# Optimization experiments

Measured on AMD Instinct MI355X. Metric: run time of the kernel, lower is better.

Reference implementation:

```python
import jax, jax.numpy as jnp
import numpy as np

MIN_D, MAX_D = 0.1, 1.0
KSIZE = 5


def gaussian_kernel(ksize):
    sigma = ksize / 6.0
    x = jnp.arange(ksize, dtype=jnp.float32) - ksize // 2
    k1 = jnp.exp(-0.5 * x ** 2 / sigma ** 2)
    k1 = k1 / k1.sum()
    return (k1[:, None] * k1[None, :])[None, None]  # [1,1,k,k]


def setup_inputs() -> dict:
    key = jax.random.key(0)
    k1, k2 = jax.random.split(key)
    B, H, W = 8, 512, 512
    TH = TW = 512
    contrast_map = jax.random.normal(k1, (B, 1, H, W), dtype=jnp.float32)
    # uniform [0,1) randoms replacing the per-sample torch.rand calls
    rand_offsets = jax.random.uniform(k2, (B, TH, TW, 4, 2), dtype=jnp.float32)
    return {
        "contrast_map": contrast_map,
        "rand_offsets": rand_offsets,
        "smoothing_kernel": gaussian_kernel(KSIZE),
        "target_height": TH,
        "target_width": TW,
    }


def reference(contrast_map, rand_offsets, smoothing_kernel, target_height, target_width):
    B, _, H, W = contrast_map.shape
    # per-sample min-max normalization to [0,1]
    mn = contrast_map.min(axis=(1, 2, 3), keepdims=True)
    mx = contrast_map.max(axis=(1, 2, 3), keepdims=True)
    norm = jnp.where(mx > mn, (contrast_map - mn) / (mx - mn), jnp.zeros_like(contrast_map))
    # gaussian smoothing, same padding
    pad = KSIZE // 2
    smoothed = jax.lax.conv_general_dilated(
        norm, smoothing_kernel, window_strides=(1, 1),
        padding=[(pad, pad), (pad, pad)],
        dimension_numbers=("NCHW", "OIHW", "NCHW"))
    # contrast -> density: min_d + (max_d-min_d) * sqrt(c)
    density = MIN_D + (MAX_D - MIN_D) * jnp.sqrt(smoothed)  # [B,1,H,W]

    # nearest-index lookup:  h_idx = floor(i*H/TH) clamped
    hi = jnp.minimum((jnp.arange(target_height) * H) // target_height, H - 1)
    wi = jnp.minimum((jnp.arange(target_width) * W) // target_width, W - 1)
    local = density[:, 0][:, hi][:, :, wi]  # [B,TH,TW]

    # per-pixel sample count: >0.7 -> 4, >0.4 -> 2, else 1
    num_samples = jnp.where(local > 0.7, 4, jnp.where(local > 0.4, 2, 1))  # int [B,TH,TW]

    yb = jnp.linspace(-1.0, 1.0, target_height)
    xb = jnp.linspace(-1.0, 1.0, target_width)
    base = jnp.stack(jnp.broadcast_arrays(yb[:, None], xb[None, :]), axis=-1)  # [TH,TW,2] (y,x)
    cell = jnp.array([2.0 / target_height, 2.0 / target_width], dtype=jnp.float32)
    off = (rand_offsets - 0.5) * cell * 0.8  # [B,TH,TW,4,2]
    use_off = (num_samples > 1)[..., None, None]  # single-sample pixels use the base coord
    coords = base[None, :, :, None, :] + jnp.where(use_off, off, 0.0)  # [B,TH,TW,4,2]

    slot = jnp.arange(4)
    valid = slot[None, None, None, :] < num_samples[..., None]  # [B,TH,TW,4]
    weights = jnp.where(valid, local[..., None] / num_samples[..., None], 0.0)  # [B,TH,TW,4]
    return coords, weights, density
```

## Files before the change

kernel.cpp:

```cpp
#include <hip/hip_runtime.h>

static constexpr int B = 8, Himg = 512, Wimg = 512, TH = 512, TW = 512;
static constexpr int BPB = 32;

typedef float f4 __attribute__((ext_vector_type(4)));
typedef float f2 __attribute__((ext_vector_type(2)));

__global__ __launch_bounds__(256) void minmax_kernel(const float* __restrict__ cm,
                                                     float* __restrict__ wsmin,
                                                     float* __restrict__ wsmax) {
    int b   = blockIdx.x / BPB;
    int blk = blockIdx.x % BPB;
    const f4* p = (const f4*)(cm + (size_t)b * Himg * Wimg);
    float mn = 3.4e38f, mx = -3.4e38f;
    int base = blk * 2048;
    #pragma unroll
    for (int k = 0; k < 8; ++k) {
        f4 v = p[base + k * 256 + threadIdx.x];
        mn = fminf(mn, fminf(fminf(v.x, v.y), fminf(v.z, v.w)));
        mx = fmaxf(mx, fmaxf(fmaxf(v.x, v.y), fmaxf(v.z, v.w)));
    }
    #pragma unroll
    for (int off = 32; off; off >>= 1) {
        mn = fminf(mn, __shfl_xor(mn, off));
        mx = fmaxf(mx, __shfl_xor(mx, off));
    }
    __shared__ float smn[4], smx[4];
    int wave = threadIdx.x >> 6, lane = threadIdx.x & 63;
    if (lane == 0) { smn[wave] = mn; smx[wave] = mx; }
    __syncthreads();
    if (threadIdx.x == 0) {
        mn = fminf(fminf(smn[0], smn[1]), fminf(smn[2], smn[3]));
        mx = fmaxf(fmaxf(smx[0], smx[1]), fmaxf(smx[2], smx[3]));
        wsmin[b * BPB + blk] = mn;
        wsmax[b * BPB + blk] = mx;
    }
}

__global__ __launch_bounds__(256) void fused_kernel(const float* __restrict__ cm,
                                                    const float* __restrict__ kern,
                                                    const float* __restrict__ wsmin,
                                                    const float* __restrict__ wsmax,
                                                    const float* __restrict__ rnd,
                                                    float* __restrict__ coords,
                                                    float* __restrict__ weights,
                                                    float* __restrict__ dens) {
    __shared__ float tile[36][37];
    __shared__ float kf[25];
    __shared__ float dsm[1024];

    int tid = threadIdx.x;
    int b = blockIdx.z;
    int bx = blockIdx.x * 32, by = blockIdx.y * 32;

    if (tid < 25) kf[tid] = kern[tid];

    float mnf = 3.4e38f, mxf = -3.4e38f;
    #pragma unroll
    for (int k = 0; k < BPB; ++k) {
        mnf = fminf(mnf, wsmin[b * BPB + k]);
        mxf = fmaxf(mxf, wsmax[b * BPB + k]);
    }
    bool ok = mxf > mnf;
    double mn = (double)mnf;
    double inv = ok ? (1.0 / ((double)mxf - mn)) : 0.0;
    float mnf32 = mnf;
    float invf32 = (float)inv;

    const float* img = cm + (size_t)b * Himg * Wimg;
    for (int idx = tid; idx < 36 * 36; idx += 256) {
        int r = idx / 36, c = idx % 36;
        int gy = by + r - 2, gx = bx + c - 2;
        float v = 0.0f;
        if (gy >= 0 && gy < Himg && gx >= 0 && gx < Wimg)
            v = ok ? (img[gy * Wimg + gx] - mnf32) * invf32 : 0.0f;
        tile[r][c] = v;
    }
    __syncthreads();

    {
        int ox = tid & 31;
        int oy0 = (tid >> 5) << 2;
        float acc[4] = {0.f, 0.f, 0.f, 0.f};
        #pragma unroll
        for (int yy = 0; yy < 8; ++yy) {
            float rv[5];
            #pragma unroll
            for (int dx = 0; dx < 5; ++dx) rv[dx] = tile[oy0 + yy][ox + dx];
            #pragma unroll
            for (int r = 0; r < 4; ++r) {
                int dy = yy - r;
                if (dy >= 0 && dy < 5) {
                    #pragma unroll
                    for (int dx = 0; dx < 5; ++dx)
                        acc[r] = fmaf(rv[dx], kf[dy * 5 + dx], acc[r]);
                }
            }
        }
        #pragma unroll
        for (int r = 0; r < 4; ++r) {
            int oy = oy0 + r;
            float D32 = 0.1f + 0.9f * sqrtf(fmaxf(acc[r], 0.0f));
            float Dout = D32;
            int code;
            if (fabsf(D32 - 0.7f) < 1e-4f || fabsf(D32 - 0.4f) < 1e-4f) {
                double s64 = 0.0;
                #pragma unroll
                for (int dy = 0; dy < 5; ++dy)
                    for (int dx = 0; dx < 5; ++dx) {
                        int gy = by + oy + dy - 2, gx = bx + ox + dx - 2;
                        double v = 0.0;
                        if (gy >= 0 && gy < Himg && gx >= 0 && gx < Wimg)
                            v = ((double)img[gy * Wimg + gx] - mn) * inv;
                        s64 += v * (double)kern[dy * 5 + dx];
                    }
                double D64 = 0.1 + 0.9 * sqrt(s64);
                code = D64 > 0.7 ? 2 : (D64 > 0.4 ? 1 : 0);
                Dout = (float)D64;
            } else {
                code = D32 > 0.7f ? 2 : (D32 > 0.4f ? 1 : 0);
            }
            unsigned u = (__float_as_uint(Dout) & ~3u) | (unsigned)code;
            float enc = __uint_as_float(u);
            dsm[oy * 32 + ox] = enc;
            dens[(size_t)b * Himg * Wimg + (size_t)(by + oy) * Wimg + (bx + ox)] = enc;
        }
    }
    __syncthreads();

    const float cy = (2.0f / TH) * 0.8f;
    const float cx = (2.0f / TW) * 0.8f;
    int lane = tid & 63, wv = tid >> 6;
    #pragma unroll
    for (int k = 0; k < 8; ++k) {
        int row = k * 4 + wv;
        int gy = by + row;
        int gx = bx + (lane >> 1);
        int h = lane & 1;

        float local = dsm[row * 32 + (lane >> 1)];
        int code = __float_as_uint(local) & 3;
        int num = 1 << code;
        bool useoff = num > 1;

        float yb = -1.0f + gy * (2.0f / (TH - 1));
        float xb = -1.0f + gx * (2.0f / (TW - 1));

        size_t f4i = 2 * ((size_t)b * (Himg * Wimg) + (size_t)gy * Wimg + bx) + lane;
        f4 r = ((const f4*)rnd)[f4i];
        f4 c;
        c.x = yb + (useoff ? (r.x - 0.5f) * cy : 0.0f);
        c.y = xb + (useoff ? (r.y - 0.5f) * cx : 0.0f);
        c.z = yb + (useoff ? (r.z - 0.5f) * cy : 0.0f);
        c.w = xb + (useoff ? (r.w - 0.5f) * cx : 0.0f);
        ((f4*)coords)[f4i] = c;

        float invw = local * __uint_as_float(0x3f800000u - ((unsigned)code << 23));
        f2 w;
        if (h == 0) {
            w.x = invw;
            w.y = (num > 1) ? invw : 0.0f;
        } else {
            float v = (num > 3) ? invw : 0.0f;
            w.x = v;
            w.y = v;
        }
        ((f2*)weights)[f4i] = w;
    }
}

extern "C" void kernel_launch(void* const* d_in, const int* in_sizes, int n_in,
                              void* d_out, int out_size, void* d_ws, size_t ws_size,
                              hipStream_t stream) {
    const float* cm   = (const float*)d_in[0];
    const float* rnd  = (const float*)d_in[1];
    const float* kern = (const float*)d_in[2];
    float* out     = (float*)d_out;
    float* coords  = out;
    float* weights = out + (size_t)B * TH * TW * 8;
    float* dens    = weights + (size_t)B * TH * TW * 4;
    float* wsmin   = (float*)d_ws;
    float* wsmax   = wsmin + B * BPB;

    minmax_kernel<<<B * BPB, 256, 0, stream>>>(cm, wsmin, wsmax);
    dim3 gridF(Wimg / 32, Himg / 32, B);
    fused_kernel<<<gridF, 256, 0, stream>>>(cm, kern, wsmin, wsmax, rnd,
                                            coords, weights, dens);
}
```

Baseline: 49.27 us.

## Split fused kernel into density stencil and flat streaming output kernel

Breaks the fused kernel into a tiled density/stencil kernel that writes the encoded density, and a separate flat 1D kernel that reads density back and streams coords and weights with full-width vector stores. The aim is simpler, fully coalesced, sync-free streaming with better occupancy for the bandwidth-bound output. In exchange it adds a kernel launch and a re-read of the density array from memory or L2.

```diff
diff --git a/kernel.cpp b/kernel.cpp
--- a/kernel.cpp
+++ b/kernel.cpp
@@ -1,10 +1,12 @@
 #include <hip/hip_runtime.h>
 
 static constexpr int B = 8, Himg = 512, Wimg = 512, TH = 512, TW = 512;
+static constexpr int NPIX = B * Himg * Wimg;
 static constexpr int BPB = 32;
+static constexpr int WBLOCKS = NPIX / 256;
+static constexpr int CBLOCKS = 2 * NPIX / 256;
 
 typedef float f4 __attribute__((ext_vector_type(4)));
-typedef float f2 __attribute__((ext_vector_type(2)));
 
 __global__ __launch_bounds__(256) void minmax_kernel(const float* __restrict__ cm,
                                                      float* __restrict__ wsmin,
@@ -37,17 +39,13 @@
     }
 }
 
-__global__ __launch_bounds__(256) void fused_kernel(const float* __restrict__ cm,
-                                                    const float* __restrict__ kern,
-                                                    const float* __restrict__ wsmin,
-                                                    const float* __restrict__ wsmax,
-                                                    const float* __restrict__ rnd,
-                                                    float* __restrict__ coords,
-                                                    float* __restrict__ weights,
-                                                    float* __restrict__ dens) {
+__global__ __launch_bounds__(256) void density_kernel(const float* __restrict__ cm,
+                                                      const float* __restrict__ kern,
+                                                      const float* __restrict__ wsmin,
+                                                      const float* __restrict__ wsmax,
+                                                      float* __restrict__ dens) {
     __shared__ float tile[36][37];
     __shared__ float kf[25];
-    __shared__ float dsm[1024];
 
     int tid = threadIdx.x;
     int b = blockIdx.z;
@@ -78,94 +76,89 @@
     }
     __syncthreads();
 
-    {
-        int ox = tid & 31;
-        int oy0 = (tid >> 5) << 2;
-        float acc[4] = {0.f, 0.f, 0.f, 0.f};
+    int ox = tid & 31;
+    int oy0 = (tid >> 5) << 2;
+    float acc[4] = {0.f, 0.f, 0.f, 0.f};
+    #pragma unroll
+    for (int yy = 0; yy < 8; ++yy) {
+        float rv[5];
         #pragma unroll
-        for (int yy = 0; yy < 8; ++yy) {
-            float rv[5];
-            #pragma unroll
-            for (int dx = 0; dx < 5; ++dx) rv[dx] = tile[oy0 + yy][ox + dx];
-            #pragma unroll
-            for (int r = 0; r < 4; ++r) {
-                int dy = yy - r;
-                if (dy >= 0 && dy < 5) {
-                    #pragma unroll
-                    for (int dx = 0; dx < 5; ++dx)
-                        acc[r] = fmaf(rv[dx], kf[dy * 5 + dx], acc[r]);
-                }
+        for (int dx = 0; dx < 5; ++dx) rv[dx] = tile[oy0 + yy][ox + dx];
+        #pragma unroll
+        for (int r = 0; r < 4; ++r) {
+            int dy = yy - r;
+            if (dy >= 0 && dy < 5) {
+                #pragma unroll
+                for (int dx = 0; dx < 5; ++dx)
+                    acc[r] = fmaf(rv[dx], kf[dy * 5 + dx], acc[r]);
             }
         }
-        #pragma unroll
-        for (int r = 0; r < 4; ++r) {
-            int oy = oy0 + r;
-            float D32 = 0.1f + 0.9f * sqrtf(fmaxf(acc[r], 0.0f));
-            float Dout = D32;
-            int code;
-            if (fabsf(D32 - 0.7f) < 1e-4f || fabsf(D32 - 0.4f) < 1e-4f) {
-                double s64 = 0.0;
-                #pragma unroll
-                for (int dy = 0; dy < 5; ++dy)
-                    for (int dx = 0; dx < 5; ++dx) {
-                        int gy = by + oy + dy - 2, gx = bx + ox + dx - 2;
-                        double v = 0.0;
-                        if (gy >= 0 && gy < Himg && gx >= 0 && gx < Wimg)
-                            v = ((double)img[gy * Wimg + gx] - mn) * inv;
-                        s64 += v * (double)kern[dy * 5 + dx];
-                    }
-                double D64 = 0.1 + 0.9 * sqrt(s64);
-                code = D64 > 0.7 ? 2 : (D64 > 0.4 ? 1 : 0);
-                Dout = (float)D64;
-            } else {
-                code = D32 > 0.7f ? 2 : (D32 > 0.4f ? 1 : 0);
-            }
-            unsigned u = (__float_as_uint(Dout) & ~3u) | (unsigned)code;
-            float enc = __uint_as_float(u);
-            dsm[oy * 32 + ox] = enc;
-            dens[(size_t)b * Himg * Wimg + (size_t)(by + oy) * Wimg + (bx + ox)] = enc;
+    }
+    #pragma unroll
+    for (int r = 0; r < 4; ++r) {
+        int oy = oy0 + r;
+        float D32 = 0.1f + 0.9f * sqrtf(fmaxf(acc[r], 0.0f));
+        float Dout = D32;
+        int code;
+        if (fabsf(D32 - 0.7f) < 1e-4f || fabsf(D32 - 0.4f) < 1e-4f) {
+            double s64 = 0.0;
+            #pragma unroll
+            for (int dy = 0; dy < 5; ++dy)
+                for (int dx = 0; dx < 5; ++dx) {
+                    int gy = by + oy + dy - 2, gx = bx + ox + dx - 2;
+                    double v = 0.0;
+                    if (gy >= 0 && gy < Himg && gx >= 0 && gx < Wimg)
+                        v = ((double)img[gy * Wimg + gx] - mn) * inv;
+                    s64 += v * (double)kern[dy * 5 + dx];
+                }
+            double D64 = 0.1 + 0.9 * sqrt(s64);
+            code = D64 > 0.7 ? 2 : (D64 > 0.4 ? 1 : 0);
+            Dout = (float)D64;
+        } else {
+            code = D32 > 0.7f ? 2 : (D32 > 0.4f ? 1 : 0);
         }
+        unsigned u = (__float_as_uint(Dout) & ~3u) | (unsigned)code;
+        dens[(size_t)b * Himg * Wimg + (size_t)(by + oy) * Wimg + (bx + ox)] =
+            __uint_as_float(u);
     }
-    __syncthreads();
+}
 
-    const float cy = (2.0f / TH) * 0.8f;
-    const float cx = (2.0f / TW) * 0.8f;
-    int lane = tid & 63, wv = tid >> 6;
-    #pragma unroll
-    for (int k = 0; k < 8; ++k) {
-        int row = k * 4 + wv;
-        int gy = by + row;
-        int gx = bx + (lane >> 1);
-        int h = lane & 1;
-
-        float local = dsm[row * 32 + (lane >> 1)];
+__global__ __launch_bounds__(256) void stream_kernel(const float* __restrict__ rnd,
+                                                     const float* __restrict__ dens,
+                                                     float* __restrict__ coords,
+                                                     float* __restrict__ weights) {
+    int bid = blockIdx.x;
+    if (bid < WBLOCKS) {
+        int p = bid * 256 + threadIdx.x;
+        float local = dens[p];
         int code = __float_as_uint(local) & 3;
         int num = 1 << code;
-        bool useoff = num > 1;
+        float invw = local * __uint_as_float(0x3f800000u - ((unsigned)code << 23));
+        f4 w;
+        w.x = invw;
+        w.y = (num > 1) ? invw : 0.0f;
+        w.z = (num > 3) ? invw : 0.0f;
+        w.w = w.z;
+        ((f4*)weights)[p] = w;
+    } else {
+        int t = (bid - WBLOCKS) * 256 + threadIdx.x;
+        int p = t >> 1;
+        float local = dens[p];
+        bool useoff = (__float_as_uint(local) & 3) != 0;
 
-        float yb = -1.0f + gy * (2.0f / (TH - 1));
-        float xb = -1.0f + gx * (2.0f / (TW - 1));
+        int rem = p & (Himg * Wimg - 1);
+        float yb = -1.0f + (rem >> 9) * (2.0f / (TH - 1));
+        float xb = -1.0f + (rem & 511) * (2.0f / (TW - 1));
+        const float cy = (2.0f / TH) * 0.8f;
+        const float cx = (2.0f / TW) * 0.8f;
 
-        size_t f4i = 2 * ((size_t)b * (Himg * Wimg) + (size_t)gy * Wimg + bx) + lane;
-        f4 r = ((const f4*)rnd)[f4i];
+        f4 r = ((const f4*)rnd)[t];
         f4 c;
         c.x = yb + (useoff ? (r.x - 0.5f) * cy : 0.0f);
         c.y = xb + (useoff ? (r.y - 0.5f) * cx : 0.0f);
         c.z = yb + (useoff ? (r.z - 0.5f) * cy : 0.0f);
         c.w = xb + (useoff ? (r.w - 0.5f) * cx : 0.0f);
-        ((f4*)coords)[f4i] = c;
-
-        float invw = local * __uint_as_float(0x3f800000u - ((unsigned)code << 23));
-        f2 w;
-        if (h == 0) {
-            w.x = invw;
-            w.y = (num > 1) ? invw : 0.0f;
-        } else {
-            float v = (num > 3) ? invw : 0.0f;
-            w.x = v;
-            w.y = v;
-        }
-        ((f2*)weights)[f4i] = w;
+        ((f4*)coords)[t] = c;
     }
 }
 
@@ -183,7 +176,7 @@
     float* wsmax   = wsmin + B * BPB;
 
     minmax_kernel<<<B * BPB, 256, 0, stream>>>(cm, wsmin, wsmax);
-    dim3 gridF(Wimg / 32, Himg / 32, B);
-    fused_kernel<<<gridF, 256, 0, stream>>>(cm, kern, wsmin, wsmax, rnd,
-                                            coords, weights, dens);
+    dim3 gridD(Wimg / 32, Himg / 32, B);
+    density_kernel<<<gridD, 256, 0, stream>>>(cm, kern, wsmin, wsmax, dens);
+    stream_kernel<<<WBLOCKS + CBLOCKS, 256, 0, stream>>>(rnd, dens, coords, weights);
 }
```

New measurement: 59.20 us. +20.1%, slower.
